# Kernel optimization log

Hardware: AMD Instinct MI355X
Metric: run time of the kernel (lower is better)

The kernel has to match this reference:

```python
import jax, jax.numpy as jnp
import numpy as np

MAX_OBJECTS = 20
NODE_DIM = 16
HIDDEN = 64
N_OPS = 8
N_COLORS = 10
B = 65536


def _lin(x, w, b):
    # torch nn.Linear: w is [out, in]
    return x @ w.T + b


def _ln(x, g, b, eps=1e-5):
    mu = x.mean(-1, keepdims=True)
    var = ((x - mu) ** 2).mean(-1, keepdims=True)
    return (x - mu) / jnp.sqrt(var + eps) * g + b


def setup_inputs() -> dict:
    key = jax.random.key(0)
    ks = jax.random.split(key, 32)
    s = 0.1
    d = {
        'node_feats': jax.random.normal(ks[0], (B, MAX_OBJECTS, NODE_DIM), jnp.float32),
        'n_nodes': jax.random.randint(ks[1], (B,), 1, MAX_OBJECTS + 1).astype(jnp.int32),
        'rnn_state': jax.random.normal(ks[2], (B, HIDDEN), jnp.float32),
        'prev_op_onehot': jnp.zeros((B, N_OPS), jnp.float32),
        'ne_w': jax.random.normal(ks[3], (HIDDEN, NODE_DIM)) * s,
        'ne_b': jnp.zeros((HIDDEN,)),
        'mp1_w1': jax.random.normal(ks[4], (HIDDEN, 2 * HIDDEN)) * s,
        'mp1_b1': jnp.zeros((HIDDEN,)),
        'mp1_w2': jax.random.normal(ks[5], (HIDDEN, HIDDEN)) * s,
        'mp1_b2': jnp.zeros((HIDDEN,)),
        'n1_g': jnp.ones((HIDDEN,)),
        'n1_b': jnp.zeros((HIDDEN,)),
        'mp2_w1': jax.random.normal(ks[6], (HIDDEN, 2 * HIDDEN)) * s,
        'mp2_b1': jnp.zeros((HIDDEN,)),
        'mp2_w2': jax.random.normal(ks[7], (HIDDEN, HIDDEN)) * s,
        'mp2_b2': jnp.zeros((HIDDEN,)),
        'n2_g': jnp.ones((HIDDEN,)),
        'n2_b': jnp.zeros((HIDDEN,)),
        'gru_wih': jax.random.normal(ks[8], (3 * HIDDEN, HIDDEN + N_OPS)) * s,
        'gru_whh': jax.random.normal(ks[9], (3 * HIDDEN, HIDDEN)) * s,
        'gru_bih': jnp.zeros((3 * HIDDEN,)),
        'gru_bhh': jnp.zeros((3 * HIDDEN,)),
        'op_w': jax.random.normal(ks[10], (N_OPS, HIDDEN)) * s,
        'op_b': jnp.zeros((N_OPS,)),
        'c1_w': jax.random.normal(ks[11], (N_COLORS, HIDDEN)) * s,
        'c1_b': jnp.zeros((N_COLORS,)),
        'c2_w': jax.random.normal(ks[12], (N_COLORS, HIDDEN)) * s,
        'c2_b': jnp.zeros((N_COLORS,)),
        'pq_w': jax.random.normal(ks[13], (HIDDEN, HIDDEN)) * s,
        'pq_b': jnp.zeros((HIDDEN,)),
        'pk_w': jax.random.normal(ks[14], (HIDDEN, HIDDEN)) * s,
        'pk_b': jnp.zeros((HIDDEN,)),
    }
    return d


def _forward(node_feats, n_nodes, rnn_state, prev_op_onehot,
             ne_w, ne_b, mp1_w1, mp1_b1, mp1_w2, mp1_b2, n1_g, n1_b,
             mp2_w1, mp2_b1, mp2_w2, mp2_b2, n2_g, n2_b,
             gru_wih, gru_whh, gru_bih, gru_bhh,
             op_w, op_b, c1_w, c1_b, c2_w, c2_b, pq_w, pq_b, pk_w, pk_b):
    # ---- encode_graph ----
    h = _lin(node_feats, ne_w, ne_b)                                   # [B, N, H]
    mask = jnp.arange(MAX_OBJECTS)[None, :] < n_nodes[:, None]         # [B, N]
    mf = mask.astype(h.dtype)[..., None]                               # [B, N, 1]
    cnt = jnp.clip(mf.sum(1, keepdims=True), 1.0)                      # [B, 1, 1]
    msg = (h * mf).sum(1, keepdims=True) / cnt                         # [B, 1, H]
    x1 = jnp.concatenate([h, jnp.broadcast_to(msg, h.shape)], -1)
    h = h + _lin(jax.nn.relu(_lin(x1, mp1_w1, mp1_b1)), mp1_w2, mp1_b2)
    h = _ln(h, n1_g, n1_b) * mf
    msg = (h * mf).sum(1, keepdims=True) / cnt
    x2 = jnp.concatenate([h, jnp.broadcast_to(msg, h.shape)], -1)
    h = h + _lin(jax.nn.relu(_lin(x2, mp2_w1, mp2_b1)), mp2_w2, mp2_b2)
    h = _ln(h, n2_g, n2_b) * mf
    graph_vec = (h * mf).sum(1) / jnp.clip(mf.sum(1), 1.0)             # [B, H]
    # ---- step (GRUCell + heads + pointer) ----
    x = jnp.concatenate([graph_vec, prev_op_onehot], -1)               # [B, H+n_ops]
    gi = x @ gru_wih.T + gru_bih                                       # [B, 3H]
    gh = rnn_state @ gru_whh.T + gru_bhh                               # [B, 3H]
    H = HIDDEN
    r = jax.nn.sigmoid(gi[:, :H] + gh[:, :H])
    z = jax.nn.sigmoid(gi[:, H:2 * H] + gh[:, H:2 * H])
    n = jnp.tanh(gi[:, 2 * H:] + r * gh[:, 2 * H:])
    new_state = (1.0 - z) * n + z * rnn_state                          # [B, H]
    op_logits = _lin(new_state, op_w, op_b)
    c1_logits = _lin(new_state, c1_w, c1_b)
    c2_logits = _lin(new_state, c2_w, c2_b)
    query = _lin(new_state, pq_w, pq_b)[:, None, :]                    # [B, 1, H]
    keys = _lin(h, pk_w, pk_b)                                         # [B, N, H]
    ptr_logits = (query * keys).sum(-1)                                # [B, N]
    ptr_logits = jnp.where(mask, ptr_logits, jnp.asarray(-1e9, ptr_logits.dtype))
    return op_logits, c1_logits, c2_logits, ptr_logits, new_state


def reference(node_feats, n_nodes, rnn_state, prev_op_onehot,
              ne_w, ne_b, mp1_w1, mp1_b1, mp1_w2, mp1_b2, n1_g, n1_b,
              mp2_w1, mp2_b1, mp2_w2, mp2_b2, n2_g, n2_b,
              gru_wih, gru_whh, gru_bih, gru_bhh,
              op_w, op_b, c1_w, c1_b, c2_w, c2_b, pq_w, pq_b, pk_w, pk_b):
    return _forward(node_feats, n_nodes, rnn_state, prev_op_onehot,
                    ne_w, ne_b, mp1_w1, mp1_b1, mp1_w2, mp1_b2, n1_g, n1_b,
                    mp2_w1, mp2_b1, mp2_w2, mp2_b2, n2_g, n2_b,
                    gru_wih, gru_whh, gru_bih, gru_bhh,
                    op_w, op_b, c1_w, c1_b, c2_w, c2_b, pq_w, pq_b, pk_w, pk_b)
```

## Files before the change

### kernel.cpp

```cpp
#include <hip/hip_runtime.h>
#include <hip/hip_bf16.h>
#include <cstdint>

#define NM 20
#define NBIN 20
#define MAXB 65536

typedef __attribute__((ext_vector_type(8))) short bf16x8;
typedef __attribute__((ext_vector_type(4))) float f32x4;
typedef __attribute__((ext_vector_type(4))) unsigned int u32x4;

union FU { bf16x8 h; u32x4 u; };

#define MFMA(A, Bf, C) __builtin_amdgcn_mfma_f32_16x16x32_bf16((A), (Bf), (C), 0, 0, 0)

#define F_NE    0
#define F_M1W1  2048
#define F_M1W2  10240
#define F_M2W1  14336
#define F_M2W2  22528
#define F_WIH   26624
#define F_WHH   45056
#define F_PQ    57344
#define F_PK    61440
#define F_PACK  65536
#define F_BNE   67584
#define F_B11   67648
#define F_B12   67712
#define F_G1    67776
#define F_L1    67840
#define F_B21   67904
#define F_B22   67968
#define F_G2    68032
#define F_L2    68096
#define F_TOTAL 68160

__device__ __align__(16) short g_fr[F_TOTAL];
__device__ __align__(16) float g_grb[4][64];
__device__ int g_hist[NBIN];
__device__ int g_off[NBIN];
__device__ int g_done;
__device__ int g_perm[MAXB];

__device__ __forceinline__ short bf16rn(float x) {
  unsigned u = __float_as_uint(x);
  u += 0x7fffu + ((u >> 16) & 1u);
  return (short)(u >> 16);
}
__device__ __forceinline__ float bf2f(short s) {
  return __uint_as_float(((unsigned)(unsigned short)s) << 16);
}
__device__ __forceinline__ unsigned pk2(float lo, float hi) {
  __hip_bfloat162 t = __float22bfloat162_rn(float2{lo, hi});
  return *reinterpret_cast<unsigned*>(&t);
}
__device__ __forceinline__ int s64(int r) {
  int mb = r >> 4, qq = (r >> 2) & 3, i = r & 3;
  return (mb >> 1) * 32 + qq * 8 + (mb & 1) * 4 + i;
}

#define LDF(off) (*(const bf16x8*)(g_fr + (off) + lane * 8))
#define LDB(off, c) (*(const bf16x8*)(g_fr + (off) + (c) * 32 + q * 8))
#define LDFz(off, z) (*(const bf16x8*)(g_fr + (off) + lane * 8 + (z)))
#define LDBz(off, c, z) (*(const bf16x8*)(g_fr + (off) + (c) * 32 + q * 8 + (z)))

#define BUILDA(OFS, MB, KC, ROWX, GET)                                 \
  for (int idx = t; idx < (MB) * (KC) * 512; idx += T) {               \
    int j = idx & 7, ln = (idx >> 3) & 63, f = idx >> 9;               \
    int mb = f / (KC), kc = f % (KC);                                  \
    int m = mb * 16 + (ln & 15);                                       \
    int k = kc * 32 + (ln >> 4) * 8 + j;                               \
    int row = (ROWX);                                                  \
    (void)row; (void)k; (void)m;                                       \
    g_fr[(OFS) + idx] = bf16rn(GET);                                   \
  }

__global__ void __launch_bounds__(256)
prep_frag(const float* __restrict__ ne_w,
          const float* __restrict__ m1w1, const float* __restrict__ m1w2,
          const float* __restrict__ m2w1, const float* __restrict__ m2w2,
          const float* __restrict__ wih,  const float* __restrict__ whh,
          const float* __restrict__ pqw,  const float* __restrict__ opw,
          const float* __restrict__ c1w,  const float* __restrict__ c2w,
          const float* __restrict__ pkw,
          const float* __restrict__ ne_b,
          const float* __restrict__ m1b1, const float* __restrict__ m1b2,
          const float* __restrict__ n1g,  const float* __restrict__ n1b,
          const float* __restrict__ m2b1, const float* __restrict__ m2b2,
          const float* __restrict__ n2g,  const float* __restrict__ n2b,
          const float* __restrict__ bih,  const float* __restrict__ bhh)
{
  const int t = blockIdx.x * blockDim.x + threadIdx.x;
  const int T = gridDim.x * blockDim.x;
  if (blockIdx.x == 0 && threadIdx.x < NBIN) g_hist[threadIdx.x] = 0;
  if (blockIdx.x == 0 && threadIdx.x == 0) g_done = 0;
  BUILDA(F_NE,   4, 1, s64(m), (k < 16 ? ne_w[row * 16 + k] : (k == 16 ? ne_b[row] : 0.f)))
  BUILDA(F_M1W1, 4, 4, s64(m), m1w1[row * 128 + k])
  BUILDA(F_M1W2, 4, 2, s64(m), m1w2[row * 64 + k])
  BUILDA(F_M2W1, 4, 4, s64(m), m2w1[row * 128 + k])
  BUILDA(F_M2W2, 4, 2, s64(m), m2w2[row * 64 + k])
  BUILDA(F_WIH, 12, 3, (m & 0xC0) | s64(m & 63), (k < 72 ? wih[row * 72 + k] : 0.f))
  BUILDA(F_WHH, 12, 2, (m & 0xC0) | s64(m & 63), whh[row * 64 + k])
  BUILDA(F_PQ,   4, 2, m, pqw[row * 64 + k])
  BUILDA(F_PK,   4, 2, m, pkw[row * 64 + k])
  BUILDA(F_PACK, 2, 2, m, (row < 8 ? opw[row * 64 + k]
                           : row < 18 ? c1w[(row - 8) * 64 + k]
                           : row < 28 ? c2w[(row - 18) * 64 + k] : 0.f))
  for (int i = t; i < 64; i += T) {
    g_fr[F_BNE + i] = bf16rn(ne_b[i]);
    g_fr[F_B11 + i] = bf16rn(m1b1[i]);
    g_fr[F_B12 + i] = bf16rn(m1b2[i]);
    g_fr[F_G1  + i] = bf16rn(n1g[i]);
    g_fr[F_L1  + i] = bf16rn(n1b[i]);
    g_fr[F_B21 + i] = bf16rn(m2b1[i]);
    g_fr[F_B22 + i] = bf16rn(m2b2[i]);
    g_fr[F_G2  + i] = bf16rn(n2g[i]);
    g_fr[F_L2  + i] = bf16rn(n2b[i]);
    g_grb[0][i] = bih[i]       + bhh[i];
    g_grb[1][i] = bih[64 + i]  + bhh[64 + i];
    g_grb[2][i] = bih[128 + i];
    g_grb[3][i] = bhh[128 + i];
  }
}

__global__ void __launch_bounds__(256)
nn_hist(const int* __restrict__ nnp, int B)
{
  __shared__ int lh[NBIN];
  __shared__ int lastdone;
  const int t = threadIdx.x;
  if (t < NBIN) lh[t] = 0;
  __syncthreads();
  for (int i = blockIdx.x * blockDim.x + t; i < B; i += gridDim.x * blockDim.x)
    atomicAdd(&lh[nnp[i] - 1], 1);
  __syncthreads();
  if (t < NBIN && lh[t] > 0) atomicAdd(&g_hist[t], lh[t]);
  __threadfence();
  if (t == 0) lastdone = (atomicAdd(&g_done, 1) == (int)gridDim.x - 1);
  __syncthreads();
  if (t == 0 && lastdone) {
    int acc = 0;
    for (int i = 0; i < NBIN; i++) { g_off[i] = acc; acc += g_hist[i]; }
  }
}

__global__ void __launch_bounds__(256)
nn_scatter(const int* __restrict__ nnp, int B)
{
  __shared__ int lc[NBIN], lbase[NBIN];
  const int t = threadIdx.x;
  const int i = blockIdx.x * 256 + t;
  if (t < NBIN) lc[t] = 0;
  __syncthreads();
  int bin = 0, r = 0;
  const bool ok = (i < B);
  if (ok) { bin = nnp[i] - 1; r = atomicAdd(&lc[bin], 1); }
  __syncthreads();
  if (t < NBIN) lbase[t] = (lc[t] > 0) ? atomicAdd(&g_off[t], lc[t]) : 0;
  __syncthreads();
  if (ok) g_perm[lbase[bin] + r] = i;
}

__device__ __forceinline__ void pack8(FU& f, const float* v) {
  f.u[0] = pk2(v[0], v[1]); f.u[1] = pk2(v[2], v[3]);
  f.u[2] = pk2(v[4], v[5]); f.u[3] = pk2(v[6], v[7]);
}

__device__ __forceinline__ void mp_stage(
    FU hA[][2], const FU* msgf,
    int w1off, int w2off, int b1o, int b2o, int lgo, int lbo,
    int nnv, int wv, int nact, int lane, int q)
{
  if (nact == 0) return;
  const f32x4 zf4 = {0.f, 0.f, 0.f, 0.f};
  f32x4 tmsg[4];
  #pragma unroll
  for (int mb = 0; mb < 4; mb++) {
    tmsg[mb] = MFMA(LDF(w1off + (mb * 4 + 2) * 512), msgf[0].h, zf4);
    tmsg[mb] = MFMA(LDF(w1off + (mb * 4 + 3) * 512), msgf[1].h, tmsg[mb]);
  }
  {
    FU b1p0, b1p1; b1p0.h = LDB(b1o, 0); b1p1.h = LDB(b1o, 1);
    #pragma unroll
    for (int mb = 0; mb < 4; mb++)
      #pragma unroll
      for (int i = 0; i < 4; i++)
        tmsg[mb][i] += bf2f(((mb >> 1) ? b1p1 : b1p0).h[(mb & 1) * 4 + i]);
  }

  #pragma unroll
  for (int t = 0; t < 5; t++) {
    if (t < nact) {
      int tz = 0;
      asm volatile("" : "+v"(tz));
      const int n = wv + 4 * t;
      f32x4 T[4];
      #pragma unroll
      for (int mb = 0; mb < 4; mb++) {
        T[mb] = MFMA(LDFz(w1off + (mb * 4 + 0) * 512, tz), hA[t][0].h, tmsg[mb]);
        T[mb] = MFMA(LDFz(w1off + (mb * 4 + 1) * 512, tz), hA[t][1].h, T[mb]);
      }
      FU tb[2];
      #pragma unroll
      for (int c = 0; c < 2; c++)
        #pragma unroll
        for (int w = 0; w < 4; w++) {
          int mb = 2 * c + (w >> 1), i0 = (w & 1) * 2;
          float lo = fmaxf(T[mb][i0],     0.f);
          float hi = fmaxf(T[mb][i0 + 1], 0.f);
          tb[c].u[w] = pk2(lo, hi);
        }
      f32x4 H[4];
      #pragma unroll
      for (int mb = 0; mb < 4; mb++) {
        H[mb] = MFMA(LDFz(w2off + (mb * 2 + 0) * 512, tz), tb[0].h, zf4);
        H[mb] = MFMA(LDFz(w2off + (mb * 2 + 1) * 512, tz), tb[1].h, H[mb]);
      }
      FU b2p0, b2p1;
      b2p0.h = LDBz(b2o, 0, tz); b2p1.h = LDBz(b2o, 1, tz);
      float y[16]; float s = 0.f, ss = 0.f;
      #pragma unroll
      for (int k = 0; k < 16; k++) {
        int c = k >> 3, j = k & 7;
        float v = H[2 * c + (j >> 2)][j & 3] + bf2f((c ? b2p1 : b2p0).h[j]) +
                  bf2f(hA[t][c].h[j]);
        y[k] = v; s += v; ss += v * v;
      }
      s += __shfl_xor(s, 16, 64); ss += __shfl_xor(ss, 16, 64);
      s += __shfl_xor(s, 32, 64); ss += __shfl_xor(ss, 32, 64);
      float mu = s * 0.015625f;
      float rstd = rsqrtf(ss * 0.015625f - mu * mu + 1e-5f);
      float mfv = (n < nnv) ? 1.f : 0.f;
      FU lgp0, lgp1, lbp0, lbp1;
      lgp0.h = LDBz(lgo, 0, tz); lgp1.h = LDBz(lgo, 1, tz);
      lbp0.h = LDBz(lbo, 0, tz); lbp1.h = LDBz(lbo, 1, tz);
      #pragma unroll
      for (int k = 0; k < 16; k++) {
        int c = k >> 3, j = k & 7;
        float hv = ((y[k] - mu) * rstd * bf2f((c ? lgp1 : lgp0).h[j]) +
                    bf2f((c ? lbp1 : lbp0).h[j])) * mfv;
        y[k] = hv;
      }
      pack8(hA[t][0], y); pack8(hA[t][1], y + 8);
    }
  }
}

__global__ void __launch_bounds__(256)
msp(const float* __restrict__ nf, const int* __restrict__ nnp,
    const float* __restrict__ rnn, const float* __restrict__ poh,
    const float* __restrict__ opb, const float* __restrict__ c1b,
    const float* __restrict__ c2b, const float* __restrict__ pqb,
    const float* __restrict__ pkb,
    float* __restrict__ out, int B)
{
  __shared__ __align__(16) float exch[2][4][64][17];
  __shared__ __align__(16) unsigned nsx[64][8];

  const int tid = threadIdx.x;
  const int wv = tid >> 6;
  const int lane = tid & 63;
  const int l15 = lane & 15, q = lane >> 4;
  const int b0 = blockIdx.x * 16;
  const int bb = g_perm[b0 + l15];

  const int nnv = nnp[bb];
  const float inv = 1.0f / (float)nnv;
  const f32x4 zf4 = {0.f, 0.f, 0.f, 0.f};

  int M = nnv;
  { int o;
    o = __shfl_xor(M, 1, 64); M = M > o ? M : o;
    o = __shfl_xor(M, 2, 64); M = M > o ? M : o;
    o = __shfl_xor(M, 4, 64); M = M > o ? M : o;
    o = __shfl_xor(M, 8, 64); M = M > o ? M : o; }
  int nact = (M - wv + 3) >> 2;
  nact = nact < 0 ? 0 : (nact > 5 ? 5 : nact);

  FU hA[5][2];
  #pragma unroll
  for (int t5 = 0; t5 < 5; t5++)
    #pragma unroll
    for (int c = 0; c < 2; c++) {
      hA[t5][c].u[0] = 0; hA[t5][c].u[1] = 0;
      hA[t5][c].u[2] = 0; hA[t5][c].u[3] = 0;
    }

  {
    #pragma unroll
    for (int t = 0; t < 5; t++) {
      if (t < nact) {
        int tz = 0;
        asm volatile("" : "+v"(tz));
        const int n = wv + 4 * t;
        FU bx;
        bx.u[0] = 0; bx.u[1] = 0; bx.u[2] = 0; bx.u[3] = 0;
        if (q < 2) {
          const float* p = nf + ((size_t)bb * NM + n) * 16 + q * 8;
          float4 x0 = *(const float4*)p, x1 = *(const float4*)(p + 4);
          bx.u[0] = pk2(x0.x, x0.y); bx.u[1] = pk2(x0.z, x0.w);
          bx.u[2] = pk2(x1.x, x1.y); bx.u[3] = pk2(x1.z, x1.w);
        } else if (q == 2) {
          bx.u[0] = pk2(1.f, 0.f);
        }
        f32x4 C[4];
        #pragma unroll
        for (int mb = 0; mb < 4; mb++) C[mb] = MFMA(LDFz(F_NE + mb * 512, tz), bx.h, zf4);
        float hv[16];
        #pragma unroll
        for (int k = 0; k < 16; k++) {
          int c = k >> 3, j = k & 7;
          hv[k] = C[2 * c + (j >> 2)][j & 3];
        }
        pack8(hA[t][0], hv); pack8(hA[t][1], hv + 8);
      }
    }
  }

  FU msgf[2];
  #define EXCHANGE(REG)                                                        \
    {                                                                          \
      _Pragma("unroll")                                                        \
      for (int k = 0; k < 16; k++) {                                           \
        int c = k >> 3, j = k & 7;                                             \
        float sK = 0.f;                                                        \
        _Pragma("unroll")                                                      \
        for (int t5 = 0; t5 < 5; t5++) {                                       \
          float vv = bf2f(hA[t5][c].h[j]);                                     \
          sK += (wv + 4 * t5 < nnv) ? vv : 0.f;                                \
        }                                                                      \
        exch[REG][wv][lane][k] = sK;                                           \
      }                                                                        \
      __syncthreads();                                                         \
      _Pragma("unroll")                                                        \
      for (int w8 = 0; w8 < 8; w8++) {                                         \
        int k0 = 2 * w8, k1 = k0 + 1;                                          \
        float a = (exch[REG][0][lane][k0] + exch[REG][1][lane][k0] +           \
                   exch[REG][2][lane][k0] + exch[REG][3][lane][k0]) * inv;     \
        float b = (exch[REG][0][lane][k1] + exch[REG][1][lane][k1] +           \
                   exch[REG][2][lane][k1] + exch[REG][3][lane][k1]) * inv;     \
        FU* dp = (w8 < 4) ? &msgf[0] : &msgf[1];                               \
        dp->u[w8 & 3] = pk2(a, b);                                             \
      }                                                                        \
    }

  EXCHANGE(0)
  mp_stage(hA, msgf, F_M1W1, F_M1W2, F_B11, F_B12, F_G1, F_L1, nnv, wv, nact, lane, q);

  EXCHANGE(1)
  mp_stage(hA, msgf, F_M2W1, F_M2W2, F_B21, F_B22, F_G2, F_L2, nnv, wv, nact, lane, q);

  EXCHANGE(0)

  {
    FU px;
    if (q == 0) {
      const float* pp = poh + (size_t)bb * 8;
      float4 p0 = *(const float4*)pp, p1 = *(const float4*)(pp + 4);
      px.u[0] = pk2(p0.x, p0.y); px.u[1] = pk2(p0.z, p0.w);
      px.u[2] = pk2(p1.x, p1.y); px.u[3] = pk2(p1.z, p1.w);
    } else { px.u[0] = 0; px.u[1] = 0; px.u[2] = 0; px.u[3] = 0; }
    const float* rr0 = rnn + (size_t)bb * 64;
    float rv[16];
    #pragma unroll
    for (int c = 0; c < 2; c++) {
      float4 a0 = *(const float4*)(rr0 + c * 32 + q * 8);
      float4 a1 = *(const float4*)(rr0 + c * 32 + q * 8 + 4);
      rv[c * 8 + 0] = a0.x; rv[c * 8 + 1] = a0.y; rv[c * 8 + 2] = a0.z; rv[c * 8 + 3] = a0.w;
      rv[c * 8 + 4] = a1.x; rv[c * 8 + 5] = a1.y; rv[c * 8 + 6] = a1.z; rv[c * 8 + 7] = a1.w;
    }
    FU ah[2]; pack8(ah[0], rv); pack8(ah[1], rv + 8);

    const int tt = wv;
    f32x4 R = MFMA(LDF(F_WIH + (tt * 3 + 0) * 512), msgf[0].h, zf4);
    R = MFMA(LDF(F_WIH + (tt * 3 + 1) * 512), msgf[1].h, R);
    R = MFMA(LDF(F_WIH + (tt * 3 + 2) * 512), px.h, R);
    R = MFMA(LDF(F_WHH + (tt * 2 + 0) * 512), ah[0].h, R);
    R = MFMA(LDF(F_WHH + (tt * 2 + 1) * 512), ah[1].h, R);
    f32x4 Z = MFMA(LDF(F_WIH + ((4 + tt) * 3 + 0) * 512), msgf[0].h, zf4);
    Z = MFMA(LDF(F_WIH + ((4 + tt) * 3 + 1) * 512), msgf[1].h, Z);
    Z = MFMA(LDF(F_WIH + ((4 + tt) * 3 + 2) * 512), px.h, Z);
    Z = MFMA(LDF(F_WHH + ((4 + tt) * 2 + 0) * 512), ah[0].h, Z);
    Z = MFMA(LDF(F_WHH + ((4 + tt) * 2 + 1) * 512), ah[1].h, Z);
    f32x4 Ni = MFMA(LDF(F_WIH + ((8 + tt) * 3 + 0) * 512), msgf[0].h, zf4);
    Ni = MFMA(LDF(F_WIH + ((8 + tt) * 3 + 1) * 512), msgf[1].h, Ni);
    Ni = MFMA(LDF(F_WIH + ((8 + tt) * 3 + 2) * 512), px.h, Ni);
    f32x4 Nh = MFMA(LDF(F_WHH + ((8 + tt) * 2 + 0) * 512), ah[0].h, zf4);
    Nh = MFMA(LDF(F_WHH + ((8 + tt) * 2 + 1) * 512), ah[1].h, Nh);

    const int dbase = q * 8 + (tt >> 1) * 32 + (tt & 1) * 4;
    f32x4 brv = *(const f32x4*)&g_grb[0][dbase];
    f32x4 bzv = *(const f32x4*)&g_grb[1][dbase];
    f32x4 bnv = *(const f32x4*)&g_grb[2][dbase];
    f32x4 bhv = *(const f32x4*)&g_grb[3][dbase];
    float nsv[4];
    #pragma unroll
    for (int i = 0; i < 4; i++) {
      const int K = (tt >> 1) * 32 + (tt & 1) * 4 + i;
      const int d = q * 8 + K;
      float rr = 1.f / (1.f + expf(-(R[i] + brv[i])));
      float zz = 1.f / (1.f + expf(-(Z[i] + bzv[i])));
      float ng = tanhf(Ni[i] + bnv[i] + rr * (Nh[i] + bhv[i]));
      float st = rv[(tt >> 1) * 8 + (tt & 1) * 4 + i];
      float v = (1.f - zz) * ng + zz * st;
      out[(size_t)B * 48 + (size_t)bb * 64 + d] = v;
      nsv[i] = v;
    }
    const int dw = (tt >> 1) * 4 + (tt & 1) * 2;
    nsx[lane][dw]     = pk2(nsv[0], nsv[1]);
    nsx[lane][dw + 1] = pk2(nsv[2], nsv[3]);
  }
  __syncthreads();

  {
    FU an0, an1;
    an0.u = *(const u32x4*)&nsx[lane][0];
    an1.u = *(const u32x4*)&nsx[lane][4];
    float qv[16];
    #pragma unroll
    for (int mb = 0; mb < 4; mb++) {
      f32x4 Qc = MFMA(LDF(F_PQ + (mb * 2 + 0) * 512), an0.h, zf4);
      Qc = MFMA(LDF(F_PQ + (mb * 2 + 1) * 512), an1.h, Qc);
      f32x4 pq4 = *(const f32x4*)&pqb[mb * 16 + q * 4];
      #pragma unroll
      for (int i = 0; i < 4; i++) qv[mb * 4 + i] = Qc[i] + pq4[i];
    }
    float qb = 0.f;
    #pragma unroll
    for (int mb = 0; mb < 4; mb++) {
      f32x4 pk4 = *(const f32x4*)&pkb[mb * 16 + q * 4];
      #pragma unroll
      for (int i = 0; i < 4; i++) qb += qv[mb * 4 + i] * pk4[i];
    }
    qb += __shfl_xor(qb, 16, 64); qb += __shfl_xor(qb, 32, 64);

    if (wv < 2) {
      f32x4 L = MFMA(LDF(F_PACK + (wv * 2 + 0) * 512), an0.h, zf4);
      L = MFMA(LDF(F_PACK + (wv * 2 + 1) * 512), an1.h, L);
      #pragma unroll
      for (int i = 0; i < 4; i++) {
        int o = wv * 16 + q * 4 + i;
        if (o < 8)       out[(size_t)bb * 8 + o] = L[i] + opb[o];
        else if (o < 18) out[(size_t)B * 8 + (size_t)bb * 10 + (o - 8)] = L[i] + c1b[o - 8];
        else if (o < 28) out[(size_t)B * 18 + (size_t)bb * 10 + (o - 18)] = L[i] + c2b[o - 18];
      }
    }
    #pragma unroll
    for (int t = 0; t < 5; t++) {
      const int n = wv + 4 * t;
      if (t < nact) {
        int tz = 0;
        asm volatile("" : "+v"(tz));
        float dt = 0.f;
        #pragma unroll
        for (int mb = 0; mb < 4; mb++) {
          f32x4 Kc = MFMA(LDFz(F_PK + (mb * 2 + 0) * 512, tz), hA[t][0].h, zf4);
          Kc = MFMA(LDFz(F_PK + (mb * 2 + 1) * 512, tz), hA[t][1].h, Kc);
          #pragma unroll
          for (int i = 0; i < 4; i++) dt += qv[mb * 4 + i] * Kc[i];
        }
        dt += __shfl_xor(dt, 16, 64); dt += __shfl_xor(dt, 32, 64);
        if (q == 0)
          out[(size_t)B * 28 + (size_t)bb * 20 + n] = (n < nnv) ? (dt + qb) : -1e9f;
      } else {
        if (q == 0)
          out[(size_t)B * 28 + (size_t)bb * 20 + n] = -1e9f;
      }
    }
  }
}

extern "C" void kernel_launch(void* const* d_in, const int* in_sizes, int n_in,
                              void* d_out, int out_size, void* d_ws, size_t ws_size,
                              hipStream_t stream)
{
  (void)n_in; (void)out_size; (void)d_ws; (void)ws_size;
  const float* nf   = (const float*)d_in[0];
  const int*   nnp  = (const int*)  d_in[1];
  const float* rnn  = (const float*)d_in[2];
  const float* poh  = (const float*)d_in[3];
  const float* ne_w = (const float*)d_in[4];
  const float* ne_b = (const float*)d_in[5];
  const float* m1w1 = (const float*)d_in[6];
  const float* m1b1 = (const float*)d_in[7];
  const float* m1w2 = (const float*)d_in[8];
  const float* m1b2 = (const float*)d_in[9];
  const float* n1g  = (const float*)d_in[10];
  const float* n1b  = (const float*)d_in[11];
  const float* m2w1 = (const float*)d_in[12];
  const float* m2b1 = (const float*)d_in[13];
  const float* m2w2 = (const float*)d_in[14];
  const float* m2b2 = (const float*)d_in[15];
  const float* n2g  = (const float*)d_in[16];
  const float* n2b  = (const float*)d_in[17];
  const float* wih  = (const float*)d_in[18];
  const float* whh  = (const float*)d_in[19];
  const float* bih  = (const float*)d_in[20];
  const float* bhh  = (const float*)d_in[21];
  const float* opw  = (const float*)d_in[22];
  const float* opb  = (const float*)d_in[23];
  const float* c1w  = (const float*)d_in[24];
  const float* c1b  = (const float*)d_in[25];
  const float* c2w  = (const float*)d_in[26];
  const float* c2b  = (const float*)d_in[27];
  const float* pqw  = (const float*)d_in[28];
  const float* pqb  = (const float*)d_in[29];
  const float* pkw  = (const float*)d_in[30];
  const float* pkb  = (const float*)d_in[31];
  float* out = (float*)d_out;
  const int B = in_sizes[1];

  prep_frag<<<132, 256, 0, stream>>>(ne_w, m1w1, m1w2, m2w1, m2w2,
                                     wih, whh, pqw, opw, c1w, c2w, pkw,
                                     ne_b, m1b1, m1b2, n1g, n1b,
                                     m2b1, m2b2, n2g, n2b, bih, bhh);
  nn_hist<<<256, 256, 0, stream>>>(nnp, B);
  nn_scatter<<<(B + 255) / 256, 256, 0, stream>>>(nnp, B);
  msp<<<B / 16, 256, 0, stream>>>(nf, nnp, rnn, poh,
                                  opb, c1b, c2b,
                                  pqb, pkb, out, B);
}
```

Before: 419.1 us.

## Hoist node feature loads, fast GRU activations, descending bin order, simplify masking

Several micro-changes land together. Per-lane fragment base pointers are hoisted out of the MFMA weight-load macros. All node-feature global loads are issued before the embedding MFMAs, and padded node masking moves into the embedding so the mean-pool sum drops its per-node predicate. The GRU sigmoid and tanh now use __expf with the hardware reciprocal, trading a little accuracy for cheaper math, and the histogram offsets are built in descending order so blocks with many nodes are scheduled first.

```diff
diff --git a/kernel.cpp b/kernel.cpp
--- a/kernel.cpp
+++ b/kernel.cpp
@@ -54,6 +54,12 @@
   __hip_bfloat162 t = __float22bfloat162_rn(float2{lo, hi});
   return *reinterpret_cast<unsigned*>(&t);
 }
+__device__ __forceinline__ float fsig(float x) {
+  return __builtin_amdgcn_rcpf(1.f + __expf(-x));
+}
+__device__ __forceinline__ float ftanh(float x) {
+  return 1.f - 2.f * __builtin_amdgcn_rcpf(1.f + __expf(2.f * x));
+}
 __device__ __forceinline__ int s64(int r) {
   int mb = r >> 4, qq = (r >> 2) & 3, i = r & 3;
   return (mb >> 1) * 32 + qq * 8 + (mb & 1) * 4 + i;
@@ -61,8 +67,8 @@
 
 #define LDF(off) (*(const bf16x8*)(g_fr + (off) + lane * 8))
 #define LDB(off, c) (*(const bf16x8*)(g_fr + (off) + (c) * 32 + q * 8))
-#define LDFz(off, z) (*(const bf16x8*)(g_fr + (off) + lane * 8 + (z)))
-#define LDBz(off, c, z) (*(const bf16x8*)(g_fr + (off) + (c) * 32 + q * 8 + (z)))
+#define GAF(off) (*(const bf16x8*)(gA + (off)))
+#define GBF(off, c) (*(const bf16x8*)(gB + (off) + (c) * 32))
 
 #define BUILDA(OFS, MB, KC, ROWX, GET)                                 \
   for (int idx = t; idx < (MB) * (KC) * 512; idx += T) {               \
@@ -140,7 +146,7 @@
   __syncthreads();
   if (t == 0 && lastdone) {
     int acc = 0;
-    for (int i = 0; i < NBIN; i++) { g_off[i] = acc; acc += g_hist[i]; }
+    for (int i = NBIN - 1; i >= 0; i--) { g_off[i] = acc; acc += g_hist[i]; }
   }
 }
 
@@ -193,12 +199,14 @@
     if (t < nact) {
       int tz = 0;
       asm volatile("" : "+v"(tz));
+      const short* gA = g_fr + lane * 8 + tz;
+      const short* gB = g_fr + q * 8 + tz;
       const int n = wv + 4 * t;
       f32x4 T[4];
       #pragma unroll
       for (int mb = 0; mb < 4; mb++) {
-        T[mb] = MFMA(LDFz(w1off + (mb * 4 + 0) * 512, tz), hA[t][0].h, tmsg[mb]);
-        T[mb] = MFMA(LDFz(w1off + (mb * 4 + 1) * 512, tz), hA[t][1].h, T[mb]);
+        T[mb] = MFMA(GAF(w1off + (mb * 4 + 0) * 512), hA[t][0].h, tmsg[mb]);
+        T[mb] = MFMA(GAF(w1off + (mb * 4 + 1) * 512), hA[t][1].h, T[mb]);
       }
       FU tb[2];
       #pragma unroll
@@ -213,11 +221,11 @@
       f32x4 H[4];
       #pragma unroll
       for (int mb = 0; mb < 4; mb++) {
-        H[mb] = MFMA(LDFz(w2off + (mb * 2 + 0) * 512, tz), tb[0].h, zf4);
-        H[mb] = MFMA(LDFz(w2off + (mb * 2 + 1) * 512, tz), tb[1].h, H[mb]);
+        H[mb] = MFMA(GAF(w2off + (mb * 2 + 0) * 512), tb[0].h, zf4);
+        H[mb] = MFMA(GAF(w2off + (mb * 2 + 1) * 512), tb[1].h, H[mb]);
       }
       FU b2p0, b2p1;
-      b2p0.h = LDBz(b2o, 0, tz); b2p1.h = LDBz(b2o, 1, tz);
+      b2p0.h = GBF(b2o, 0); b2p1.h = GBF(b2o, 1);
       float y[16]; float s = 0.f, ss = 0.f;
       #pragma unroll
       for (int k = 0; k < 16; k++) {
@@ -232,8 +240,8 @@
       float rstd = rsqrtf(ss * 0.015625f - mu * mu + 1e-5f);
       float mfv = (n < nnv) ? 1.f : 0.f;
       FU lgp0, lgp1, lbp0, lbp1;
-      lgp0.h = LDBz(lgo, 0, tz); lgp1.h = LDBz(lgo, 1, tz);
-      lbp0.h = LDBz(lbo, 0, tz); lbp1.h = LDBz(lbo, 1, tz);
+      lgp0.h = GBF(lgo, 0); lgp1.h = GBF(lgo, 1);
+      lbp0.h = GBF(lbo, 0); lbp1.h = GBF(lbo, 1);
       #pragma unroll
       for (int k = 0; k < 16; k++) {
         int c = k >> 3, j = k & 7;
@@ -278,41 +286,53 @@
   nact = nact < 0 ? 0 : (nact > 5 ? 5 : nact);
 
   FU hA[5][2];
-  #pragma unroll
-  for (int t5 = 0; t5 < 5; t5++)
-    #pragma unroll
-    for (int c = 0; c < 2; c++) {
-      hA[t5][c].u[0] = 0; hA[t5][c].u[1] = 0;
-      hA[t5][c].u[2] = 0; hA[t5][c].u[3] = 0;
-    }
 
   {
+    float4 xa[5][2];
+    #pragma unroll
+    for (int t = 0; t < 5; t++) {
+      if (t < nact && q < 2) {
+        const float* p = nf + ((size_t)bb * NM + (wv + 4 * t)) * 16 + q * 8;
+        xa[t][0] = *(const float4*)p;
+        xa[t][1] = *(const float4*)(p + 4);
+      }
+    }
     #pragma unroll
     for (int t = 0; t < 5; t++) {
       if (t < nact) {
         int tz = 0;
         asm volatile("" : "+v"(tz));
+        const short* gA = g_fr + lane * 8 + tz;
         const int n = wv + 4 * t;
         FU bx;
         bx.u[0] = 0; bx.u[1] = 0; bx.u[2] = 0; bx.u[3] = 0;
         if (q < 2) {
-          const float* p = nf + ((size_t)bb * NM + n) * 16 + q * 8;
-          float4 x0 = *(const float4*)p, x1 = *(const float4*)(p + 4);
-          bx.u[0] = pk2(x0.x, x0.y); bx.u[1] = pk2(x0.z, x0.w);
-          bx.u[2] = pk2(x1.x, x1.y); bx.u[3] = pk2(x1.z, x1.w);
+          bx.u[0] = pk2(xa[t][0].x, xa[t][0].y); bx.u[1] = pk2(xa[t][0].z, xa[t][0].w);
+          bx.u[2] = pk2(xa[t][1].x, xa[t][1].y); bx.u[3] = pk2(xa[t][1].z, xa[t][1].w);
         } else if (q == 2) {
           bx.u[0] = pk2(1.f, 0.f);
         }
         f32x4 C[4];
         #pragma unroll
-        for (int mb = 0; mb < 4; mb++) C[mb] = MFMA(LDFz(F_NE + mb * 512, tz), bx.h, zf4);
+        for (int mb = 0; mb < 4; mb++) C[mb] = MFMA(GAF(F_NE + mb * 512), bx.h, zf4);
+        const float mfv = (n < nnv) ? 1.f : 0.f;
         float hv[16];
         #pragma unroll
         for (int k = 0; k < 16; k++) {
           int c = k >> 3, j = k & 7;
-          hv[k] = C[2 * c + (j >> 2)][j & 3];
+          hv[k] = C[2 * c + (j >> 2)][j & 3] * mfv;
         }
         pack8(hA[t][0], hv); pack8(hA[t][1], hv + 8);
+      }
+    }
+    #pragma unroll
+    for (int t = 0; t < 5; t++) {
+      if (t >= nact) {
+        #pragma unroll
+        for (int c = 0; c < 2; c++) {
+          hA[t][c].u[0] = 0; hA[t][c].u[1] = 0;
+          hA[t][c].u[2] = 0; hA[t][c].u[3] = 0;
+        }
       }
     }
   }
@@ -323,12 +343,9 @@
       _Pragma("unroll")                                                        \
       for (int k = 0; k < 16; k++) {                                           \
         int c = k >> 3, j = k & 7;                                             \
-        float sK = 0.f;                                                        \
-        _Pragma("unroll")                                                      \
-        for (int t5 = 0; t5 < 5; t5++) {                                       \
-          float vv = bf2f(hA[t5][c].h[j]);                                     \
-          sK += (wv + 4 * t5 < nnv) ? vv : 0.f;                                \
-        }                                                                      \
+        float sK = bf2f(hA[0][c].h[j]) + bf2f(hA[1][c].h[j]) +                 \
+                   bf2f(hA[2][c].h[j]) + bf2f(hA[3][c].h[j]) +                 \
+                   bf2f(hA[4][c].h[j]);                                        \
         exch[REG][wv][lane][k] = sK;                                           \
       }                                                                        \
       __syncthreads();                                                         \
@@ -398,9 +415,9 @@
     for (int i = 0; i < 4; i++) {
       const int K = (tt >> 1) * 32 + (tt & 1) * 4 + i;
       const int d = q * 8 + K;
-      float rr = 1.f / (1.f + expf(-(R[i] + brv[i])));
-      float zz = 1.f / (1.f + expf(-(Z[i] + bzv[i])));
-      float ng = tanhf(Ni[i] + bnv[i] + rr * (Nh[i] + bhv[i]));
+      float rr = fsig(R[i] + brv[i]);
+      float zz = fsig(Z[i] + bzv[i]);
+      float ng = ftanh(Ni[i] + bnv[i] + rr * (Nh[i] + bhv[i]));
       float st = rv[(tt >> 1) * 8 + (tt & 1) * 4 + i];
       float v = (1.f - zz) * ng + zz * st;
       out[(size_t)B * 48 + (size_t)bb * 64 + d] = v;
@@ -451,11 +468,12 @@
       if (t < nact) {
         int tz = 0;
         asm volatile("" : "+v"(tz));
+        const short* gA = g_fr + lane * 8 + tz;
         float dt = 0.f;
         #pragma unroll
         for (int mb = 0; mb < 4; mb++) {
-          f32x4 Kc = MFMA(LDFz(F_PK + (mb * 2 + 0) * 512, tz), hA[t][0].h, zf4);
-          Kc = MFMA(LDFz(F_PK + (mb * 2 + 1) * 512, tz), hA[t][1].h, Kc);
+          f32x4 Kc = MFMA(GAF(F_PK + (mb * 2 + 0) * 512), hA[t][0].h, zf4);
+          Kc = MFMA(GAF(F_PK + (mb * 2 + 1) * 512), hA[t][1].h, Kc);
           #pragma unroll
           for (int i = 0; i < 4; i++) dt += qv[mb * 4 + i] * Kc[i];
         }
```

After: 401.8 us. 1.04x faster.
